# Kernel tuning notes

Hardware: AMD Instinct MI355X
Metric: run time of the kernel (lower is better)

Reference implementation:

```python
import jax, jax.numpy as jnp
import numpy as np

N = 50000
E = 800000
D = 128          # in_dim == hidden_dim
EDGE_DIM = 1
H = 128          # hidden_dim


def setup_inputs() -> dict:
    key = jax.random.key(0)
    ks = jax.random.split(key, 16)
    inp = {
        "x": jax.random.normal(ks[0], (N, D), jnp.float32),
        "pos": jax.random.normal(ks[1], (N, 3), jnp.float32),
        "edge_index": jax.random.randint(ks[2], (2, E), 0, N, jnp.int64),
        "edge_attr": jax.random.normal(ks[3], (E, EDGE_DIM), jnp.float32),
        "s": jax.random.uniform(ks[4], (N,), jnp.float32),
    }
    # edge_mlp: Linear(2D+1+edge_dim -> H), SiLU, Linear(H -> H), SiLU
    e_in = 2 * D + 1 + EDGE_DIM
    def lin(k, fan_in, fan_out):
        lim = 1.0 / np.sqrt(fan_in)
        kw, kb = jax.random.split(k)
        W = jax.random.uniform(kw, (fan_in, fan_out), jnp.float32, -lim, lim)
        b = jax.random.uniform(kb, (fan_out,), jnp.float32, -lim, lim)
        return W, b
    inp["W_e1"], inp["b_e1"] = lin(ks[5], e_in, H)
    inp["W_e2"], inp["b_e2"] = lin(ks[6], H, H)
    # node_mlp: Linear(D+H -> H), SiLU, Linear(H -> D)
    inp["W_n1"], inp["b_n1"] = lin(ks[7], D + H, H)
    inp["W_n2"], inp["b_n2"] = lin(ks[8], H, D)
    # coord_mlp: Linear(H -> 1)
    inp["W_c"], inp["b_c"] = lin(ks[9], H, 1)
    return inp


def reference(x, pos, edge_index, edge_attr, s,
              W_e1, b_e1, W_e2, b_e2, W_n1, b_n1, W_n2, b_n2, W_c, b_c):
    src, dst = edge_index[0], edge_index[1]
    n = x.shape[0]

    # edge gather + relative geometry
    diff = pos[dst] - pos[src]                      # [E, 3]
    r2 = jnp.sum(diff * diff, axis=-1, keepdims=True)  # [E, 1]
    e_in = jnp.concatenate([x[dst], x[src], r2, edge_attr], axis=-1)  # [E, 2D+1+edge_dim]

    # edge MLP
    m = jax.nn.silu(e_in @ W_e1 + b_e1)
    m = jax.nn.silu(m @ W_e2 + b_e2)                # [E, H]

    # s-gate on source nodes
    m = m * s[src][:, None]

    # scatter-add aggregation with degree normalization
    m_sum = jax.ops.segment_sum(m, dst, num_segments=n)          # [N, H]
    deg = jax.ops.segment_sum(jnp.ones((m.shape[0], 1), m.dtype), dst, num_segments=n)
    deg = jnp.maximum(deg, 1.0)
    m_sum = m_sum / deg

    # node update
    h = jax.nn.silu(jnp.concatenate([x, m_sum], axis=-1) @ W_n1 + b_n1)
    x_out = h @ W_n2 + b_n2                         # [N, D]

    # coordinate update
    gamma = m @ W_c + b_c                           # [E, 1]
    coord_update = jax.ops.segment_sum(gamma * diff, dst, num_segments=n) / deg
    pos_out = pos + coord_update                    # [N, 3]
    return x_out, pos_out
```

## Files before the change

kernel.cpp:

```cpp
#include <hip/hip_runtime.h>
#include <hip/hip_bf16.h>

#define NN 50000
#define EE 800000
#define SCAN_BLOCKS 196

typedef __bf16 bf16x8_t __attribute__((ext_vector_type(8)));
typedef float f32x4_t __attribute__((ext_vector_type(4)));

__device__ __forceinline__ float silu_f(float v) {
    return v * __builtin_amdgcn_rcpf(1.0f + __expf(-v));
}

__device__ __forceinline__ float bf_lo(unsigned u) { return __uint_as_float(u << 16); }
__device__ __forceinline__ float bf_hi(unsigned u) { return __uint_as_float(u & 0xffff0000u); }

__global__ void prep_kernel(const float* __restrict__ x,
                            const float* __restrict__ We1,
                            const float* __restrict__ We2,
                            const float* __restrict__ Wn1,
                            const float* __restrict__ Wn2,
                            const int* __restrict__ eidx,
                            __bf16* __restrict__ xb,
                            __bf16* __restrict__ WyS,
                            __bf16* __restrict__ We2S,
                            __bf16* __restrict__ Wn1T,
                            __bf16* __restrict__ Wn2T,
                            int* __restrict__ hist) {
    int tid = blockIdx.x * blockDim.x + threadIdx.x;
    int np = gridDim.x * blockDim.x;
    const int NX = NN * 128 / 4;
    for (int i = tid; i < NX; i += np) {
        float4 v = ((const float4*)x)[i];
        __bf16* o = xb + (size_t)i * 4;
        o[0] = (__bf16)v.x; o[1] = (__bf16)v.y; o[2] = (__bf16)v.z; o[3] = (__bf16)v.w;
    }
    for (int i = tid; i < 256 * 128; i += np) {
        int k = i >> 7, n = i & 127;
        int h = (k < 128) ? n : (128 + n);
        int k2 = k & 127;
        WyS[(k2 >> 5) * 8192 + h * 32 + (k2 & 31)] = (__bf16)We1[i];
        Wn1T[n * 256 + k] = (__bf16)Wn1[i];
    }
    for (int i = tid; i < 128 * 128; i += np) {
        int k = i >> 7, n = i & 127;
        We2S[(k >> 5) * 4096 + n * 32 + (k & 31)] = (__bf16)We2[i];
        Wn2T[n * 128 + k] = (__bf16)Wn2[i];
    }
    for (int i = tid; i < EE; i += np) {
        atomicAdd(&hist[eidx[EE + i]], 1);
    }
}

__global__ __launch_bounds__(256, 3)
void ygemm_kernel(const __bf16* __restrict__ xb,
                  const __bf16* __restrict__ WyS,
                  __bf16* __restrict__ ya,
                  __bf16* __restrict__ yb) {
    __shared__ __align__(16) __bf16 Wy[256 * 32];

    const int t = threadIdx.x;
    const int r0 = blockIdx.x * 64;
    const int w = t >> 6;
    const int lane = t & 63;
    const int m_ = lane & 15;
    const int q = lane >> 4;

    const int node = r0 + w * 16 + m_;
    const long nrow = (long)(node < NN ? node : NN - 1) * 128;

    f32x4_t acc[16];
#pragma unroll
    for (int ot = 0; ot < 16; ++ot) acc[ot] = (f32x4_t){0.f, 0.f, 0.f, 0.f};

    const int wrow = t >> 2;
    const int pch = (t & 3) ^ ((wrow >> 1) & 3);
    const int wofs = wrow * 32 + pch * 8;
    const int rofs = m_ * 32 + (q ^ ((m_ >> 1) & 3)) * 8;

    bf16x8_t xf = *(const bf16x8_t*)(xb + nrow + q * 8);
    uint4 v0 = *(const uint4*)(WyS + t * 8);
    uint4 v1 = *(const uint4*)(WyS + 2048 + t * 8);
    uint4 v2 = *(const uint4*)(WyS + 4096 + t * 8);
    uint4 v3 = *(const uint4*)(WyS + 6144 + t * 8);
#pragma unroll
    for (int ks = 0; ks < 4; ++ks) {
        __syncthreads();
        *(uint4*)(Wy + wofs) = v0;
        *(uint4*)(Wy + 64 * 32 + wofs) = v1;
        *(uint4*)(Wy + 128 * 32 + wofs) = v2;
        *(uint4*)(Wy + 192 * 32 + wofs) = v3;
        __syncthreads();
        bf16x8_t nxf;
        if (ks < 3) {
            v0 = *(const uint4*)(WyS + (ks + 1) * 8192 + t * 8);
            v1 = *(const uint4*)(WyS + (ks + 1) * 8192 + 2048 + t * 8);
            v2 = *(const uint4*)(WyS + (ks + 1) * 8192 + 4096 + t * 8);
            v3 = *(const uint4*)(WyS + (ks + 1) * 8192 + 6144 + t * 8);
            nxf = *(const bf16x8_t*)(xb + nrow + (ks + 1) * 32 + q * 8);
        }
#pragma unroll
        for (int ot = 0; ot < 16; ++ot) {
            bf16x8_t wf = *(const bf16x8_t*)(Wy + ot * (16 * 32) + rofs);
            acc[ot] = __builtin_amdgcn_mfma_f32_16x16x32_bf16(wf, xf, acc[ot], 0, 0, 0);
        }
        if (ks < 3) xf = nxf;
    }

    if (node < NN) {
#pragma unroll
        for (int ot = 0; ot < 16; ++ot) {
            union { __bf16 h[4]; uint2 u; } pk;
            pk.h[0] = (__bf16)acc[ot][0];
            pk.h[1] = (__bf16)acc[ot][1];
            pk.h[2] = (__bf16)acc[ot][2];
            pk.h[3] = (__bf16)acc[ot][3];
            int col = (ot & 7) * 16 + q * 4;
            __bf16* dst = (ot < 8 ? ya : yb) + (long)node * 128 + col;
            *(uint2*)dst = pk.u;
        }
    }
}

__global__ void scan_a(const int* __restrict__ hist, int* __restrict__ bsum) {
    __shared__ int sh[256];
    int i = blockIdx.x * 256 + threadIdx.x;
    sh[threadIdx.x] = (i < NN) ? hist[i] : 0;
    __syncthreads();
    for (int s = 128; s > 0; s >>= 1) {
        if (threadIdx.x < s) sh[threadIdx.x] += sh[threadIdx.x + s];
        __syncthreads();
    }
    if (threadIdx.x == 0) bsum[blockIdx.x] = sh[0];
}

__global__ void scan_b(int* __restrict__ bsum) {
    __shared__ int sh[SCAN_BLOCKS];
    int t = threadIdx.x;
    if (t < SCAN_BLOCKS) sh[t] = bsum[t];
    __syncthreads();
    if (t == 0) {
        int acc = 0;
        for (int i = 0; i < SCAN_BLOCKS; ++i) { int v = sh[i]; sh[i] = acc; acc += v; }
    }
    __syncthreads();
    if (t < SCAN_BLOCKS) bsum[t] = sh[t];
}

__global__ void scan_c(const int* __restrict__ hist, const int* __restrict__ bsum,
                       int* __restrict__ off, int* __restrict__ cursor) {
    __shared__ int sh[256];
    int tx = threadIdx.x;
    int i = blockIdx.x * 256 + tx;
    int v = (i < NN) ? hist[i] : 0;
    sh[tx] = v;
    __syncthreads();
    for (int s = 1; s < 256; s <<= 1) {
        int add = (tx >= s) ? sh[tx - s] : 0;
        __syncthreads();
        sh[tx] += add;
        __syncthreads();
    }
    int excl = sh[tx] - v + bsum[blockIdx.x];
    if (i < NN) { off[i] = excl; cursor[i] = excl; }
    if (i == NN - 1) off[NN] = excl + v;
}

__global__ void scatter_kernel(const int* __restrict__ eidx,
                               const float* __restrict__ pos,
                               const float* __restrict__ eattr,
                               const float* __restrict__ s,
                               int* __restrict__ cursor,
                               float4* __restrict__ e_geo,
                               int2* __restrict__ e_nodes,
                               float2* __restrict__ e_gate) {
    int i = blockIdx.x * blockDim.x + threadIdx.x;
    if (i < EE) {
        int si = eidx[i];
        int di = eidx[EE + i];
        int p = atomicAdd(&cursor[di], 1);
        float dx = pos[di * 3 + 0] - pos[si * 3 + 0];
        float dy = pos[di * 3 + 1] - pos[si * 3 + 1];
        float dz = pos[di * 3 + 2] - pos[si * 3 + 2];
        e_geo[p] = make_float4(dx, dy, dz, dx * dx + dy * dy + dz * dz);
        e_nodes[p] = make_int2(si, di);
        e_gate[p] = make_float2(eattr[i], s[si]);
    }
}

__global__ __launch_bounds__(256, 3)
void edge_kernel(const __bf16* __restrict__ ya,
                 const __bf16* __restrict__ yb,
                 const float4* __restrict__ e_geo,
                 const int2* __restrict__ e_nodes,
                 const float2* __restrict__ e_gate,
                 const float* __restrict__ We1,
                 const float* __restrict__ be1,
                 const __bf16* __restrict__ We2S,
                 const float* __restrict__ be2,
                 const float* __restrict__ Wc,
                 const float* __restrict__ bc,
                 float* __restrict__ msum,
                 float* __restrict__ coordsum) {
    __shared__ __align__(16) __bf16 Wt[128 * 32];
    __shared__ __align__(16) __bf16 A2[128 * 136];
    __shared__ __align__(16) float4 s_pk[128];
    __shared__ float s_sg[128], s_g[128];
    __shared__ float s_diff[128 * 3];
    __shared__ int s_dst[128];

    float* Mf = (float*)A2;

    const int t = threadIdx.x;
    const int e0 = blockIdx.x * 128;
    const int w = t >> 6;
    const int lane = t & 63;
    const int m_ = lane & 15;
    const int q = lane >> 4;

    if (t < 128) {
        float4 g = e_geo[e0 + t];
        int2 nd = e_nodes[e0 + t];
        float2 gt = e_gate[e0 + t];
        s_diff[t * 3 + 0] = g.x; s_diff[t * 3 + 1] = g.y; s_diff[t * 3 + 2] = g.z;
        s_pk[t] = make_float4(g.w, gt.x, __int_as_float(nd.x), __int_as_float(nd.y));
        s_sg[t] = gt.y;
        s_dst[t] = nd.y;
    }
    __syncthreads();

    const int el0 = w * 16 + m_;
    const int el1 = 64 + w * 16 + m_;

    {
        const int c8 = (t & 15) * 8;
        const int eb = t >> 4;
        float4 b1a = *(const float4*)(be1 + c8);
        float4 b1b = *(const float4*)(be1 + c8 + 4);
        float4 w6a = *(const float4*)(We1 + 256 * 128 + c8);
        float4 w6b = *(const float4*)(We1 + 256 * 128 + c8 + 4);
        float4 w7a = *(const float4*)(We1 + 257 * 128 + c8);
        float4 w7b = *(const float4*)(We1 + 257 * 128 + c8 + 4);
#pragma unroll 2
        for (int i = 0; i < 8; ++i) {
            int e = eb + i * 16;
            float4 pk4 = s_pk[e];
            float r2 = pk4.x, ea = pk4.y;
            int sn = __float_as_int(pk4.z);
            int dn = __float_as_int(pk4.w);
            uint4 av = *(const uint4*)(ya + (long)dn * 128 + c8);
            uint4 bv = *(const uint4*)(yb + (long)sn * 128 + c8);
            union { __bf16 h[8]; uint4 u; } pk;
            pk.h[0] = (__bf16)silu_f(bf_lo(av.x) + bf_lo(bv.x) + b1a.x + r2 * w6a.x + ea * w7a.x);
            pk.h[1] = (__bf16)silu_f(bf_hi(av.x) + bf_hi(bv.x) + b1a.y + r2 * w6a.y + ea * w7a.y);
            pk.h[2] = (__bf16)silu_f(bf_lo(av.y) + bf_lo(bv.y) + b1a.z + r2 * w6a.z + ea * w7a.z);
            pk.h[3] = (__bf16)silu_f(bf_hi(av.y) + bf_hi(bv.y) + b1a.w + r2 * w6a.w + ea * w7a.w);
            pk.h[4] = (__bf16)silu_f(bf_lo(av.z) + bf_lo(bv.z) + b1b.x + r2 * w6b.x + ea * w7b.x);
            pk.h[5] = (__bf16)silu_f(bf_hi(av.z) + bf_hi(bv.z) + b1b.y + r2 * w6b.y + ea * w7b.y);
            pk.h[6] = (__bf16)silu_f(bf_lo(av.w) + bf_lo(bv.w) + b1b.z + r2 * w6b.z + ea * w7b.z);
            pk.h[7] = (__bf16)silu_f(bf_hi(av.w) + bf_hi(bv.w) + b1b.w + r2 * w6b.w + ea * w7b.w);
            *(uint4*)(A2 + e * 136 + c8) = pk.u;
        }
    }

    f32x4_t acc[2][8];
#pragma unroll
    for (int et = 0; et < 2; ++et)
#pragma unroll
        for (int ot = 0; ot < 8; ++ot) acc[et][ot] = (f32x4_t){0.f, 0.f, 0.f, 0.f};

    const int wrow = t >> 2;
    const int pch = (t & 3) ^ ((wrow >> 1) & 3);
    const int wofs = wrow * 32 + pch * 8;
    const int rofs = m_ * 32 + (q ^ ((m_ >> 1) & 3)) * 8;

    uint4 w20 = *(const uint4*)(We2S + t * 8);
    uint4 w21 = *(const uint4*)(We2S + 2048 + t * 8);
#pragma unroll
    for (int ks = 0; ks < 4; ++ks) {
        __syncthreads();
        *(uint4*)(Wt + wofs) = w20;
        *(uint4*)(Wt + 64 * 32 + wofs) = w21;
        __syncthreads();
        if (ks < 3) {
            w20 = *(const uint4*)(We2S + (ks + 1) * 4096 + t * 8);
            w21 = *(const uint4*)(We2S + (ks + 1) * 4096 + 2048 + t * 8);
        }
        bf16x8_t af0 = *(const bf16x8_t*)(A2 + el0 * 136 + ks * 32 + q * 8);
        bf16x8_t af1 = *(const bf16x8_t*)(A2 + el1 * 136 + ks * 32 + q * 8);
#pragma unroll
        for (int ot = 0; ot < 8; ++ot) {
            bf16x8_t wf = *(const bf16x8_t*)(Wt + ot * (16 * 32) + rofs);
            acc[0][ot] = __builtin_amdgcn_mfma_f32_16x16x32_bf16(wf, af0, acc[0][ot], 0, 0, 0);
            acc[1][ot] = __builtin_amdgcn_mfma_f32_16x16x32_bf16(wf, af1, acc[1][ot], 0, 0, 0);
        }
    }

    {
        float sg0 = s_sg[el0], sg1 = s_sg[el1];
        float gp0 = 0.f, gp1 = 0.f;
#pragma unroll
        for (int ot = 0; ot < 8; ++ot) {
            int oc = ot * 16 + q * 4;
            float4 b2 = *(const float4*)(be2 + oc);
            float4 wc = *(const float4*)(Wc + oc);
            f32x4_t v0_ = acc[0][ot], v1_ = acc[1][ot];
            v0_[0] = silu_f(v0_[0] + b2.x) * sg0; v0_[1] = silu_f(v0_[1] + b2.y) * sg0;
            v0_[2] = silu_f(v0_[2] + b2.z) * sg0; v0_[3] = silu_f(v0_[3] + b2.w) * sg0;
            v1_[0] = silu_f(v1_[0] + b2.x) * sg1; v1_[1] = silu_f(v1_[1] + b2.y) * sg1;
            v1_[2] = silu_f(v1_[2] + b2.z) * sg1; v1_[3] = silu_f(v1_[3] + b2.w) * sg1;
            acc[0][ot] = v0_; acc[1][ot] = v1_;
            gp0 += v0_[0] * wc.x + v0_[1] * wc.y + v0_[2] * wc.z + v0_[3] * wc.w;
            gp1 += v1_[0] * wc.x + v1_[1] * wc.y + v1_[2] * wc.z + v1_[3] * wc.w;
        }
        gp0 += __shfl_xor(gp0, 16); gp0 += __shfl_xor(gp0, 32);
        gp1 += __shfl_xor(gp1, 16); gp1 += __shfl_xor(gp1, 32);
        if (q == 0) {
            float b0 = bc[0];
            s_g[el0] = gp0 + b0;
            s_g[el1] = gp1 + b0;
        }
    }
    __syncthreads();

    if (t < 24) {
        int ax = t % 3, ch = t / 3;
        int base = ch * 16;
        float run = 0.f;
        int cur = s_dst[base];
        for (int r = 0; r < 16; ++r) {
            int rr = base + r;
            int d = s_dst[rr];
            if (d != cur) {
                atomicAdd(&coordsum[cur * 3 + ax], run);
                run = 0.f; cur = d;
            }
            run += s_g[rr] * s_diff[rr * 3 + ax];
        }
        atomicAdd(&coordsum[cur * 3 + ax], run);
    }

#pragma unroll
    for (int ph = 0; ph < 2; ++ph) {
        int lr = w * 16 + m_;
#pragma unroll
        for (int ot = 0; ot < 8; ++ot)
            *(f32x4_t*)(Mf + lr * 132 + ot * 16 + q * 4) = acc[ph][ot];
        __syncthreads();
        {
            int c = t & 127;
            int half = t >> 7;
            int base = ph * 64 + half * 32;
            float run = 0.f;
            int cur = s_dst[base];
            for (int r = 0; r < 32; ++r) {
                int d = s_dst[base + r];
                if (d != cur) {
                    atomicAdd(&msum[(long)cur * 128 + c], run);
                    run = 0.f; cur = d;
                }
                run += Mf[(half * 32 + r) * 132 + c];
            }
            atomicAdd(&msum[(long)cur * 128 + c], run);
        }
        __syncthreads();
    }
}

__global__ __launch_bounds__(256, 2)
void node_kernel(const __bf16* __restrict__ xb,
                 const float* __restrict__ msum,
                 const int* __restrict__ off,
                 const __bf16* __restrict__ Wn1T,
                 const float* __restrict__ bn1,
                 const __bf16* __restrict__ Wn2T,
                 const float* __restrict__ bn2,
                 const float* __restrict__ pos,
                 const float* __restrict__ csum,
                 float* __restrict__ xout,
                 float* __restrict__ pout) {
    __shared__ __align__(16) __bf16 Abf[64 * 264];
    __shared__ __align__(16) __bf16 Wt[128 * 56];
    __shared__ __align__(16) __bf16 A2[64 * 136];

    const int t = threadIdx.x;
    const int r0 = blockIdx.x * 64;
    const int w = t >> 6;
    const int lane = t & 63;
    const int m_ = lane & 15;
    const int q = lane >> 4;

    if (t < 192) {
        int node = r0 + t / 3;
        if (node < NN) {
            int dg = off[node + 1] - off[node];
            float inv = 1.f / (float)(dg < 1 ? 1 : dg);
            int fl = node * 3 + t % 3;
            pout[fl] = pos[fl] + csum[fl] * inv;
        }
    }

    for (int i = 0; i < 8; ++i) {
        int id = t + 256 * i;
        int rl = id >> 5, ch = id & 31;
        int row = r0 + rl;
        int c8 = (ch & 15) * 8;
        union { __bf16 h[8]; uint4 u; } pk;
        if (row < NN) {
            if (ch < 16) {
                pk.u = *(const uint4*)(xb + (long)row * 128 + c8);
            } else {
                const float* mp = msum + (long)row * 128 + c8;
                int dg = off[row + 1] - off[row];
                float inv = 1.f / (float)(dg < 1 ? 1 : dg);
#pragma unroll
                for (int j = 0; j < 8; ++j) pk.h[j] = (__bf16)(mp[j] * inv);
            }
        } else {
            pk.u = make_uint4(0, 0, 0, 0);
        }
        *(uint4*)(Abf + rl * 264 + ((ch < 16) ? 0 : 128) + c8) = pk.u;
    }
    __syncthreads();

    f32x4_t acc[8];
#pragma unroll
    for (int ct = 0; ct < 8; ++ct) acc[ct] = (f32x4_t){0.f, 0.f, 0.f, 0.f};

    for (int ks = 0; ks < 8; ++ks) {
#pragma unroll
        for (int i = 0; i < 2; ++i) {
            int c = t + 256 * i;
            int n = c >> 2, ko = (c & 3) * 8;
            uint4 v = *(const uint4*)(Wn1T + n * 256 + ks * 32 + ko);
            *(uint4*)(Wt + n * 56 + ko) = v;
        }
        __syncthreads();
        bf16x8_t a = *(const bf16x8_t*)(Abf + (w * 16 + m_) * 264 + ks * 32 + q * 8);
#pragma unroll
        for (int ct = 0; ct < 8; ++ct) {
            bf16x8_t b = *(const bf16x8_t*)(Wt + (ct * 16 + m_) * 56 + q * 8);
            acc[ct] = __builtin_amdgcn_mfma_f32_16x16x32_bf16(a, b, acc[ct], 0, 0, 0);
        }
        __syncthreads();
    }
#pragma unroll
    for (int ct = 0; ct < 8; ++ct) {
        int c = ct * 16 + m_;
        float b1 = bn1[c];
#pragma unroll
        for (int r = 0; r < 4; ++r) {
            int el = w * 16 + q * 4 + r;
            float v = acc[ct][r] + b1;
            A2[el * 136 + c] = (__bf16)silu_f(v);
        }
    }
    __syncthreads();

#pragma unroll
    for (int ct = 0; ct < 8; ++ct) acc[ct] = (f32x4_t){0.f, 0.f, 0.f, 0.f};

    for (int ks = 0; ks < 4; ++ks) {
#pragma unroll
        for (int i = 0; i < 2; ++i) {
            int c = t + 256 * i;
            int n = c >> 2, ko = (c & 3) * 8;
            uint4 v = *(const uint4*)(Wn2T + n * 128 + ks * 32 + ko);
            *(uint4*)(Wt + n * 56 + ko) = v;
        }
        __syncthreads();
        bf16x8_t a = *(const bf16x8_t*)(A2 + (w * 16 + m_) * 136 + ks * 32 + q * 8);
#pragma unroll
        for (int ct = 0; ct < 8; ++ct) {
            bf16x8_t b = *(const bf16x8_t*)(Wt + (ct * 16 + m_) * 56 + q * 8);
            acc[ct] = __builtin_amdgcn_mfma_f32_16x16x32_bf16(a, b, acc[ct], 0, 0, 0);
        }
        __syncthreads();
    }
#pragma unroll
    for (int ct = 0; ct < 8; ++ct) {
        int c = ct * 16 + m_;
        float b2 = bn2[c];
#pragma unroll
        for (int r = 0; r < 4; ++r) {
            int el = w * 16 + q * 4 + r;
            int row = r0 + el;
            if (row < NN) xout[(long)row * 128 + c] = acc[ct][r] + b2;
        }
    }
}

extern "C" void kernel_launch(void* const* d_in, const int* in_sizes, int n_in,
                              void* d_out, int out_size, void* d_ws, size_t ws_size,
                              hipStream_t stream) {
    const float* x     = (const float*)d_in[0];
    const float* pos   = (const float*)d_in[1];
    const int*   eidx  = (const int*)d_in[2];
    const float* eattr = (const float*)d_in[3];
    const float* s     = (const float*)d_in[4];
    const float* We1   = (const float*)d_in[5];
    const float* be1   = (const float*)d_in[6];
    const float* We2   = (const float*)d_in[7];
    const float* be2   = (const float*)d_in[8];
    const float* Wn1   = (const float*)d_in[9];
    const float* bn1   = (const float*)d_in[10];
    const float* Wn2   = (const float*)d_in[11];
    const float* bn2   = (const float*)d_in[12];
    const float* Wc    = (const float*)d_in[13];
    const float* bc    = (const float*)d_in[14];

    char* ws = (char*)d_ws;
    __bf16* xb     = (__bf16*)(ws);
    __bf16* WyS    = (__bf16*)(ws + 12800000);
    __bf16* We2S   = (__bf16*)(ws + 12865536);
    __bf16* Wn1T   = (__bf16*)(ws + 12898304);
    __bf16* Wn2T   = (__bf16*)(ws + 12963840);
    float*  msum   = (float*)(ws + 12996608);
    float*  csum   = (float*)(ws + 38596608);
    int*    hist   = (int*)(ws + 39196608);
    int*    off    = (int*)(ws + 39396608);
    int*    cursor = (int*)(ws + 39596672);
    float4* e_geo  = (float4*)(ws + 39796736);
    int2*   e_nodes= (int2*)(ws + 52596736);
    float2* e_gate = (float2*)(ws + 58996736);
    int*    bsum   = (int*)(ws + 65396736);
    __bf16* ya     = (__bf16*)(ws + 65397760);
    __bf16* yb     = (__bf16*)(ws + 78197760);

    float* xout = (float*)d_out;
    float* pout = xout + (size_t)NN * 128;

    hipMemsetAsync(ws + 12996608, 0, 26400000, stream);
    prep_kernel<<<1024, 256, 0, stream>>>(x, We1, We2, Wn1, Wn2, eidx,
                                          xb, WyS, We2S, Wn1T, Wn2T, hist);
    ygemm_kernel<<<(NN + 63) / 64, 256, 0, stream>>>(xb, WyS, ya, yb);
    scan_a<<<SCAN_BLOCKS, 256, 0, stream>>>(hist, bsum);
    scan_b<<<1, 256, 0, stream>>>(bsum);
    scan_c<<<SCAN_BLOCKS, 256, 0, stream>>>(hist, bsum, off, cursor);
    scatter_kernel<<<(EE + 255) / 256, 256, 0, stream>>>(eidx, pos, eattr, s, cursor,
                                                         e_geo, e_nodes, e_gate);
    edge_kernel<<<EE / 128, 256, 0, stream>>>(ya, yb, e_geo, e_nodes, e_gate,
                                              We1, be1, We2S, be2, Wc, bc,
                                              msum, csum);
    node_kernel<<<(NN + 63) / 64, 256, 0, stream>>>(xb, msum, off, Wn1T, bn1, Wn2T, bn2,
                                                    pos, csum, xout, pout);
}
```

Baseline: 371.8 us.

## Pack edge records, prefetch edge gathers, restructure node MLP with register-resident inputs

The scatter kernel now writes one interleaved 32-byte record per edge instead of three separate arrays, so the edge kernel reads each edge with two adjacent loads. The edge kernel's first layer software-pipelines the ya/yb row gathers one iteration ahead to hide gather latency. The node kernel drops its large staged activation tile: inputs are loaded straight into registers per k-step, weights are pre-swizzled into k-slab layout with an XOR LDS pattern and double-buffered through registers, and occupancy rises to 4 blocks per SM. This adds register pressure and more complex indexing in exchange for less LDS traffic and fewer scattered loads.

```diff
diff --git a/kernel.cpp b/kernel.cpp
--- a/kernel.cpp
+++ b/kernel.cpp
@@ -24,8 +24,8 @@
                             __bf16* __restrict__ xb,
                             __bf16* __restrict__ WyS,
                             __bf16* __restrict__ We2S,
-                            __bf16* __restrict__ Wn1T,
-                            __bf16* __restrict__ Wn2T,
+                            __bf16* __restrict__ Wn1S,
+                            __bf16* __restrict__ Wn2S,
                             int* __restrict__ hist) {
     int tid = blockIdx.x * blockDim.x + threadIdx.x;
     int np = gridDim.x * blockDim.x;
@@ -40,12 +40,12 @@
         int h = (k < 128) ? n : (128 + n);
         int k2 = k & 127;
         WyS[(k2 >> 5) * 8192 + h * 32 + (k2 & 31)] = (__bf16)We1[i];
-        Wn1T[n * 256 + k] = (__bf16)Wn1[i];
+        Wn1S[(k >> 5) * 4096 + n * 32 + (k & 31)] = (__bf16)Wn1[i];
     }
     for (int i = tid; i < 128 * 128; i += np) {
         int k = i >> 7, n = i & 127;
         We2S[(k >> 5) * 4096 + n * 32 + (k & 31)] = (__bf16)We2[i];
-        Wn2T[n * 128 + k] = (__bf16)Wn2[i];
+        Wn2S[(k >> 5) * 4096 + n * 32 + (k & 31)] = (__bf16)Wn2[i];
     }
     for (int i = tid; i < EE; i += np) {
         atomicAdd(&hist[eidx[EE + i]], 1);
@@ -171,9 +171,7 @@
                                const float* __restrict__ eattr,
                                const float* __restrict__ s,
                                int* __restrict__ cursor,
-                               float4* __restrict__ e_geo,
-                               int2* __restrict__ e_nodes,
-                               float2* __restrict__ e_gate) {
+                               uint4* __restrict__ erec) {
     int i = blockIdx.x * blockDim.x + threadIdx.x;
     if (i < EE) {
         int si = eidx[i];
@@ -182,18 +180,20 @@
         float dx = pos[di * 3 + 0] - pos[si * 3 + 0];
         float dy = pos[di * 3 + 1] - pos[si * 3 + 1];
         float dz = pos[di * 3 + 2] - pos[si * 3 + 2];
-        e_geo[p] = make_float4(dx, dy, dz, dx * dx + dy * dy + dz * dz);
-        e_nodes[p] = make_int2(si, di);
-        e_gate[p] = make_float2(eattr[i], s[si]);
+        float r2 = dx * dx + dy * dy + dz * dz;
+        uint4 a = make_uint4(__float_as_uint(dx), __float_as_uint(dy),
+                             __float_as_uint(dz), __float_as_uint(r2));
+        uint4 b = make_uint4((unsigned)si, (unsigned)di,
+                             __float_as_uint(eattr[i]), __float_as_uint(s[si]));
+        erec[(size_t)p * 2] = a;
+        erec[(size_t)p * 2 + 1] = b;
     }
 }
 
 __global__ __launch_bounds__(256, 3)
 void edge_kernel(const __bf16* __restrict__ ya,
                  const __bf16* __restrict__ yb,
-                 const float4* __restrict__ e_geo,
-                 const int2* __restrict__ e_nodes,
-                 const float2* __restrict__ e_gate,
+                 const uint4* __restrict__ erec,
                  const float* __restrict__ We1,
                  const float* __restrict__ be1,
                  const __bf16* __restrict__ We2S,
@@ -219,13 +219,16 @@
     const int q = lane >> 4;
 
     if (t < 128) {
-        float4 g = e_geo[e0 + t];
-        int2 nd = e_nodes[e0 + t];
-        float2 gt = e_gate[e0 + t];
-        s_diff[t * 3 + 0] = g.x; s_diff[t * 3 + 1] = g.y; s_diff[t * 3 + 2] = g.z;
-        s_pk[t] = make_float4(g.w, gt.x, __int_as_float(nd.x), __int_as_float(nd.y));
-        s_sg[t] = gt.y;
-        s_dst[t] = nd.y;
+        const uint4* er = erec + (size_t)(e0 + t) * 2;
+        uint4 a = er[0];
+        uint4 b = er[1];
+        s_diff[t * 3 + 0] = __uint_as_float(a.x);
+        s_diff[t * 3 + 1] = __uint_as_float(a.y);
+        s_diff[t * 3 + 2] = __uint_as_float(a.z);
+        s_pk[t] = make_float4(__uint_as_float(a.w), __uint_as_float(b.z),
+                              __uint_as_float(b.x), __uint_as_float(b.y));
+        s_sg[t] = __uint_as_float(b.w);
+        s_dst[t] = (int)b.y;
     }
     __syncthreads();
 
@@ -241,15 +244,19 @@
         float4 w6b = *(const float4*)(We1 + 256 * 128 + c8 + 4);
         float4 w7a = *(const float4*)(We1 + 257 * 128 + c8);
         float4 w7b = *(const float4*)(We1 + 257 * 128 + c8 + 4);
-#pragma unroll 2
+        float4 pk4 = s_pk[eb];
+        uint4 av = *(const uint4*)(ya + (long)__float_as_int(pk4.w) * 128 + c8);
+        uint4 bv = *(const uint4*)(yb + (long)__float_as_int(pk4.z) * 128 + c8);
+#pragma unroll
         for (int i = 0; i < 8; ++i) {
+            float4 pk4n; uint4 avn, bvn;
+            if (i < 7) {
+                pk4n = s_pk[eb + (i + 1) * 16];
+                avn = *(const uint4*)(ya + (long)__float_as_int(pk4n.w) * 128 + c8);
+                bvn = *(const uint4*)(yb + (long)__float_as_int(pk4n.z) * 128 + c8);
+            }
             int e = eb + i * 16;
-            float4 pk4 = s_pk[e];
             float r2 = pk4.x, ea = pk4.y;
-            int sn = __float_as_int(pk4.z);
-            int dn = __float_as_int(pk4.w);
-            uint4 av = *(const uint4*)(ya + (long)dn * 128 + c8);
-            uint4 bv = *(const uint4*)(yb + (long)sn * 128 + c8);
             union { __bf16 h[8]; uint4 u; } pk;
             pk.h[0] = (__bf16)silu_f(bf_lo(av.x) + bf_lo(bv.x) + b1a.x + r2 * w6a.x + ea * w7a.x);
             pk.h[1] = (__bf16)silu_f(bf_hi(av.x) + bf_hi(bv.x) + b1a.y + r2 * w6a.y + ea * w7a.y);
@@ -260,6 +267,7 @@
             pk.h[6] = (__bf16)silu_f(bf_lo(av.w) + bf_lo(bv.w) + b1b.z + r2 * w6b.z + ea * w7b.z);
             pk.h[7] = (__bf16)silu_f(bf_hi(av.w) + bf_hi(bv.w) + b1b.w + r2 * w6b.w + ea * w7b.w);
             *(uint4*)(A2 + e * 136 + c8) = pk.u;
+            if (i < 7) { pk4 = pk4n; av = avn; bv = bvn; }
         }
     }
 
@@ -367,20 +375,19 @@
     }
 }
 
-__global__ __launch_bounds__(256, 2)
+__global__ __launch_bounds__(256, 4)
 void node_kernel(const __bf16* __restrict__ xb,
                  const float* __restrict__ msum,
                  const int* __restrict__ off,
-                 const __bf16* __restrict__ Wn1T,
+                 const __bf16* __restrict__ Wn1S,
                  const float* __restrict__ bn1,
-                 const __bf16* __restrict__ Wn2T,
+                 const __bf16* __restrict__ Wn2S,
                  const float* __restrict__ bn2,
                  const float* __restrict__ pos,
                  const float* __restrict__ csum,
                  float* __restrict__ xout,
                  float* __restrict__ pout) {
-    __shared__ __align__(16) __bf16 Abf[64 * 264];
-    __shared__ __align__(16) __bf16 Wt[128 * 56];
+    __shared__ __align__(16) __bf16 Wt[128 * 32];
     __shared__ __align__(16) __bf16 A2[64 * 136];
 
     const int t = threadIdx.x;
@@ -400,92 +407,105 @@
         }
     }
 
-    for (int i = 0; i < 8; ++i) {
-        int id = t + 256 * i;
-        int rl = id >> 5, ch = id & 31;
-        int row = r0 + rl;
-        int c8 = (ch & 15) * 8;
-        union { __bf16 h[8]; uint4 u; } pk;
-        if (row < NN) {
-            if (ch < 16) {
-                pk.u = *(const uint4*)(xb + (long)row * 128 + c8);
+    const int node = r0 + w * 16 + m_;
+    const int ncl = node < NN ? node : NN - 1;
+    const long nrow = (long)ncl * 128;
+    const int dg = off[ncl + 1] - off[ncl];
+    const float inv = 1.f / (float)(dg < 1 ? 1 : dg);
+
+    f32x4_t acc[8];
+#pragma unroll
+    for (int ot = 0; ot < 8; ++ot) acc[ot] = (f32x4_t){0.f, 0.f, 0.f, 0.f};
+
+    const int wrow = t >> 2;
+    const int pch = (t & 3) ^ ((wrow >> 1) & 3);
+    const int wofs = wrow * 32 + pch * 8;
+    const int rofs = m_ * 32 + (q ^ ((m_ >> 1) & 3)) * 8;
+
+    bf16x8_t xf = *(const bf16x8_t*)(xb + nrow + q * 8);
+    float4 mf0, mf1;
+    uint4 v0 = *(const uint4*)(Wn1S + t * 8);
+    uint4 v1 = *(const uint4*)(Wn1S + 2048 + t * 8);
+#pragma unroll
+    for (int ks = 0; ks < 8; ++ks) {
+        __syncthreads();
+        *(uint4*)(Wt + wofs) = v0;
+        *(uint4*)(Wt + 64 * 32 + wofs) = v1;
+        __syncthreads();
+        bf16x8_t nxf; float4 nm0, nm1;
+        if (ks < 7) {
+            v0 = *(const uint4*)(Wn1S + (ks + 1) * 4096 + t * 8);
+            v1 = *(const uint4*)(Wn1S + (ks + 1) * 4096 + 2048 + t * 8);
+            if (ks + 1 < 4) {
+                nxf = *(const bf16x8_t*)(xb + nrow + (ks + 1) * 32 + q * 8);
             } else {
-                const float* mp = msum + (long)row * 128 + c8;
-                int dg = off[row + 1] - off[row];
-                float inv = 1.f / (float)(dg < 1 ? 1 : dg);
-#pragma unroll
-                for (int j = 0; j < 8; ++j) pk.h[j] = (__bf16)(mp[j] * inv);
+                const float* mp = msum + nrow + (ks + 1 - 4) * 32 + q * 8;
+                nm0 = *(const float4*)(mp);
+                nm1 = *(const float4*)(mp + 4);
             }
+        }
+        bf16x8_t cf;
+        if (ks < 4) {
+            cf = xf;
         } else {
-            pk.u = make_uint4(0, 0, 0, 0);
-        }
-        *(uint4*)(Abf + rl * 264 + ((ch < 16) ? 0 : 128) + c8) = pk.u;
-    }
-    __syncthreads();
-
-    f32x4_t acc[8];
-#pragma unroll
-    for (int ct = 0; ct < 8; ++ct) acc[ct] = (f32x4_t){0.f, 0.f, 0.f, 0.f};
-
-    for (int ks = 0; ks < 8; ++ks) {
-#pragma unroll
-        for (int i = 0; i < 2; ++i) {
-            int c = t + 256 * i;
-            int n = c >> 2, ko = (c & 3) * 8;
-            uint4 v = *(const uint4*)(Wn1T + n * 256 + ks * 32 + ko);
-            *(uint4*)(Wt + n * 56 + ko) = v;
-        }
-        __syncthreads();
-        bf16x8_t a = *(const bf16x8_t*)(Abf + (w * 16 + m_) * 264 + ks * 32 + q * 8);
-#pragma unroll
-        for (int ct = 0; ct < 8; ++ct) {
-            bf16x8_t b = *(const bf16x8_t*)(Wt + (ct * 16 + m_) * 56 + q * 8);
-            acc[ct] = __builtin_amdgcn_mfma_f32_16x16x32_bf16(a, b, acc[ct], 0, 0, 0);
-        }
-        __syncthreads();
-    }
-#pragma unroll
-    for (int ct = 0; ct < 8; ++ct) {
-        int c = ct * 16 + m_;
-        float b1 = bn1[c];
-#pragma unroll
-        for (int r = 0; r < 4; ++r) {
-            int el = w * 16 + q * 4 + r;
-            float v = acc[ct][r] + b1;
-            A2[el * 136 + c] = (__bf16)silu_f(v);
-        }
-    }
-    __syncthreads();
-
-#pragma unroll
-    for (int ct = 0; ct < 8; ++ct) acc[ct] = (f32x4_t){0.f, 0.f, 0.f, 0.f};
-
+            union { __bf16 h[8]; bf16x8_t v; } u;
+            u.h[0] = (__bf16)(mf0.x * inv); u.h[1] = (__bf16)(mf0.y * inv);
+            u.h[2] = (__bf16)(mf0.z * inv); u.h[3] = (__bf16)(mf0.w * inv);
+            u.h[4] = (__bf16)(mf1.x * inv); u.h[5] = (__bf16)(mf1.y * inv);
+            u.h[6] = (__bf16)(mf1.z * inv); u.h[7] = (__bf16)(mf1.w * inv);
+            cf = u.v;
+        }
+#pragma unroll
+        for (int ot = 0; ot < 8; ++ot) {
+            bf16x8_t wf = *(const bf16x8_t*)(Wt + ot * (16 * 32) + rofs);
+            acc[ot] = __builtin_amdgcn_mfma_f32_16x16x32_bf16(wf, cf, acc[ot], 0, 0, 0);
+        }
+        if (ks < 7) {
+            if (ks + 1 < 4) xf = nxf;
+            else { mf0 = nm0; mf1 = nm1; }
+        }
+    }
+
+#pragma unroll
+    for (int ot = 0; ot < 8; ++ot) {
+        float4 b1 = *(const float4*)(bn1 + ot * 16 + q * 4);
+        union { __bf16 h[4]; uint2 u; } pk;
+        pk.h[0] = (__bf16)silu_f(acc[ot][0] + b1.x);
+        pk.h[1] = (__bf16)silu_f(acc[ot][1] + b1.y);
+        pk.h[2] = (__bf16)silu_f(acc[ot][2] + b1.z);
+        pk.h[3] = (__bf16)silu_f(acc[ot][3] + b1.w);
+        *(uint2*)(A2 + (w * 16 + m_) * 136 + ot * 16 + q * 4) = pk.u;
+        acc[ot] = (f32x4_t){0.f, 0.f, 0.f, 0.f};
+    }
+
+    uint4 u0 = *(const uint4*)(Wn2S + t * 8);
+    uint4 u1 = *(const uint4*)(Wn2S + 2048 + t * 8);
+#pragma unroll
     for (int ks = 0; ks < 4; ++ks) {
-#pragma unroll
-        for (int i = 0; i < 2; ++i) {
-            int c = t + 256 * i;
-            int n = c >> 2, ko = (c & 3) * 8;
-            uint4 v = *(const uint4*)(Wn2T + n * 128 + ks * 32 + ko);
-            *(uint4*)(Wt + n * 56 + ko) = v;
-        }
-        __syncthreads();
-        bf16x8_t a = *(const bf16x8_t*)(A2 + (w * 16 + m_) * 136 + ks * 32 + q * 8);
-#pragma unroll
-        for (int ct = 0; ct < 8; ++ct) {
-            bf16x8_t b = *(const bf16x8_t*)(Wt + (ct * 16 + m_) * 56 + q * 8);
-            acc[ct] = __builtin_amdgcn_mfma_f32_16x16x32_bf16(a, b, acc[ct], 0, 0, 0);
-        }
-        __syncthreads();
-    }
-#pragma unroll
-    for (int ct = 0; ct < 8; ++ct) {
-        int c = ct * 16 + m_;
-        float b2 = bn2[c];
-#pragma unroll
-        for (int r = 0; r < 4; ++r) {
-            int el = w * 16 + q * 4 + r;
-            int row = r0 + el;
-            if (row < NN) xout[(long)row * 128 + c] = acc[ct][r] + b2;
+        __syncthreads();
+        *(uint4*)(Wt + wofs) = u0;
+        *(uint4*)(Wt + 64 * 32 + wofs) = u1;
+        __syncthreads();
+        if (ks < 3) {
+            u0 = *(const uint4*)(Wn2S + (ks + 1) * 4096 + t * 8);
+            u1 = *(const uint4*)(Wn2S + (ks + 1) * 4096 + 2048 + t * 8);
+        }
+        bf16x8_t af = *(const bf16x8_t*)(A2 + (w * 16 + m_) * 136 + ks * 32 + q * 8);
+#pragma unroll
+        for (int ot = 0; ot < 8; ++ot) {
+            bf16x8_t wf = *(const bf16x8_t*)(Wt + ot * (16 * 32) + rofs);
+            acc[ot] = __builtin_amdgcn_mfma_f32_16x16x32_bf16(wf, af, acc[ot], 0, 0, 0);
+        }
+    }
+
+    if (node < NN) {
+#pragma unroll
+        for (int ot = 0; ot < 8; ++ot) {
+            float4 b2 = *(const float4*)(bn2 + ot * 16 + q * 4);
+            float4 o;
+            o.x = acc[ot][0] + b2.x; o.y = acc[ot][1] + b2.y;
+            o.z = acc[ot][2] + b2.z; o.w = acc[ot][3] + b2.w;
+            *(float4*)(xout + nrow + ot * 16 + q * 4) = o;
         }
     }
 }
@@ -513,16 +533,14 @@
     __bf16* xb     = (__bf16*)(ws);
     __bf16* WyS    = (__bf16*)(ws + 12800000);
     __bf16* We2S   = (__bf16*)(ws + 12865536);
-    __bf16* Wn1T   = (__bf16*)(ws + 12898304);
-    __bf16* Wn2T   = (__bf16*)(ws + 12963840);
+    __bf16* Wn1S   = (__bf16*)(ws + 12898304);
+    __bf16* Wn2S   = (__bf16*)(ws + 12963840);
     float*  msum   = (float*)(ws + 12996608);
     float*  csum   = (float*)(ws + 38596608);
     int*    hist   = (int*)(ws + 39196608);
     int*    off    = (int*)(ws + 39396608);
     int*    cursor = (int*)(ws + 39596672);
-    float4* e_geo  = (float4*)(ws + 39796736);
-    int2*   e_nodes= (int2*)(ws + 52596736);
-    float2* e_gate = (float2*)(ws + 58996736);
+    uint4*  erec   = (uint4*)(ws + 39796736);
     int*    bsum   = (int*)(ws + 65396736);
     __bf16* ya     = (__bf16*)(ws + 65397760);
     __bf16* yb     = (__bf16*)(ws + 78197760);
@@ -532,16 +550,15 @@
 
     hipMemsetAsync(ws + 12996608, 0, 26400000, stream);
     prep_kernel<<<1024, 256, 0, stream>>>(x, We1, We2, Wn1, Wn2, eidx,
-                                          xb, WyS, We2S, Wn1T, Wn2T, hist);
+                                          xb, WyS, We2S, Wn1S, Wn2S, hist);
     ygemm_kernel<<<(NN + 63) / 64, 256, 0, stream>>>(xb, WyS, ya, yb);
     scan_a<<<SCAN_BLOCKS, 256, 0, stream>>>(hist, bsum);
     scan_b<<<1, 256, 0, stream>>>(bsum);
     scan_c<<<SCAN_BLOCKS, 256, 0, stream>>>(hist, bsum, off, cursor);
-    scatter_kernel<<<(EE + 255) / 256, 256, 0, stream>>>(eidx, pos, eattr, s, cursor,
-                                                         e_geo, e_nodes, e_gate);
-    edge_kernel<<<EE / 128, 256, 0, stream>>>(ya, yb, e_geo, e_nodes, e_gate,
+    scatter_kernel<<<(EE + 255) / 256, 256, 0, stream>>>(eidx, pos, eattr, s, cursor, erec);
+    edge_kernel<<<EE / 128, 256, 0, stream>>>(ya, yb, erec,
                                               We1, be1, We2S, be2, Wc, bc,
                                               msum, csum);
-    node_kernel<<<(NN + 63) / 64, 256, 0, stream>>>(xb, msum, off, Wn1T, bn1, Wn2T, bn2,
+    node_kernel<<<(NN + 63) / 64, 256, 0, stream>>>(xb, msum, off, Wn1S, bn1, Wn2S, bn2,
                                                     pos, csum, xout, pout);
 }
```

Measured after the change: 347.1 us. -6.6%, faster.
